# Kernel tuning notes

Hardware: AMD Instinct MI355X
Metric: run time of the kernel (lower is better)

## Reference

```python
import jax, jax.numpy as jnp
import numpy as np
import math

CHUNK = 128  # hardcoded chunk_size in the original module


def setup_inputs() -> dict:
    key = jax.random.key(0)
    ks = jax.random.split(key, 6)
    B, C, T, H, W = 8, 256, 16, 8, 8
    KC, VC = 8192, 512  # key_channels, value_channels (dk = KC/heads = T*H*W = 1024)
    return {
        "x": jax.random.normal(ks[0], (B, C, T, H, W), dtype=jnp.float32),
        "Wk": jax.random.normal(ks[1], (KC, C), dtype=jnp.float32) * 0.02,
        "Wq": jax.random.normal(ks[2], (KC, C), dtype=jnp.float32) * 0.02,
        "Wv": jax.random.normal(ks[3], (VC, C), dtype=jnp.float32) * 0.02,
        "Wr": jax.random.normal(ks[4], (C, VC), dtype=jnp.float32) * 0.02,
        "br": jnp.zeros((C,), dtype=jnp.float32),
        "num_heads": 8,
    }


def reference(x, Wk, Wq, Wv, Wr, br, num_heads):
    B, C, T, H, W = x.shape
    N = T * H * W
    # 1x1x1 Conv3d == per-position linear projection
    k = jnp.einsum('oc,bcthw->bothw', Wk, x).reshape(B, num_heads, -1, N)
    q = jnp.einsum('oc,bcthw->bothw', Wq, x).reshape(B, num_heads, -1, N)
    v = jnp.einsum('oc,bcthw->bothw', Wv, x).reshape(B, num_heads, -1, N)
    dk = k.shape[2]  # == N by structural constraint of the original matmul
    # matmul(keys, q_chunk) over all chunks at once (matmul is linear in q):
    # contracts keys' position axis with queries' channel axis, as in torch.
    scores = jnp.matmul(k, q) / math.sqrt(dk)  # [B, h, dk, N]
    # softmax applied per query-chunk of size CHUNK along the last axis
    nchunks = N // CHUNK
    attn = jax.nn.softmax(
        scores.reshape(B, num_heads, dk, nchunks, CHUNK), axis=-1
    ).reshape(B, num_heads, dk, N)
    out = jnp.matmul(v, attn)  # [B, h, dv, N] (dk == N)
    out = out.reshape(B, -1, T, H, W)
    out = jnp.einsum('oc,bcthw->bothw', Wr, out) + br[None, :, None, None, None]
    return out
```

## Files before the change

### kernel.cpp

```cpp
#include <hip/hip_runtime.h>
#include <hip/hip_bf16.h>


using bf16x8 = __attribute__((ext_vector_type(8))) __bf16;
using f32x4  = __attribute__((ext_vector_type(4))) float;
using s16x4  = __attribute__((ext_vector_type(4))) short;

static __device__ __forceinline__ short f2b(float f) {
  union { float f; unsigned u; } v; v.f = f;
  unsigned r = v.u + 0x7fffu + ((v.u >> 16) & 1u);
  return (short)(r >> 16);
}

static __device__ __forceinline__ void gll16(const void* g, void* l) {
  __builtin_amdgcn_global_load_lds(
      (const __attribute__((address_space(1))) void*)g,
      (__attribute__((address_space(3))) void*)l, 16, 0, 0);
}

#define MFMA16(a, b, c) __builtin_amdgcn_mfma_f32_16x16x32_bf16((a), (b), (c), 0, 0, 0)

__global__ __launch_bounds__(256) void cvt_bf16(const float* __restrict__ in,
                                                short* __restrict__ out, int n) {
  int i = (blockIdx.x * 256 + threadIdx.x) * 4;
  if (i >= n) return;
  float4 v = *(const float4*)(in + i);
  s16x4 s = { f2b(v.x), f2b(v.y), f2b(v.z), f2b(v.w) };
  *(s16x4*)(out + i) = s;
}

__global__ __launch_bounds__(256) void tcvt(const float* __restrict__ in,
    short* __restrict__ outP, short* __restrict__ outT,
    int R, int C, long inB, long pB, long tB)
{
  __shared__ short tile[64][68];
  long bz = blockIdx.z;
  const float* src = in + bz * inB;
  int r0 = blockIdx.y * 64, c0 = blockIdx.x * 64;
  int t = threadIdx.x;
  int r = t >> 2, cq = (t & 3) * 16;
  #pragma unroll
  for (int e = 0; e < 16; e += 4) {
    float4 v = *(const float4*)(&src[(long)(r0 + r) * C + (c0 + cq + e)]);
    s16x4 s = { f2b(v.x), f2b(v.y), f2b(v.z), f2b(v.w) };
    *(s16x4*)(&tile[r][cq + e]) = s;
    if (outP) *(s16x4*)(&outP[bz * pB + (long)(r0 + r) * C + (c0 + cq + e)]) = s;
  }
  __syncthreads();
  int tr = t >> 2, re = (t & 3) * 16;
  short tmp[16];
  #pragma unroll
  for (int e = 0; e < 16; ++e) tmp[e] = tile[re + e][tr];
  short* dst = &outT[bz * tB + (long)(c0 + tr) * R + (r0 + re)];
  #pragma unroll
  for (int e = 0; e < 16; e += 4) *(s16x4*)(&dst[e]) = *(const s16x4*)(&tmp[e]);
}

template<bool F32OUT>
__global__ __launch_bounds__(256) void gemm_nt(
    const short* __restrict__ A, const short* __restrict__ B,
    void* __restrict__ C, const float* __restrict__ bias,
    int M, int N, int K, int lda, int ldb, int ldc,
    long aSB, long aSH, long bSB, long bSH, long cSB, long cSH, int nh)
{
  int batch = blockIdx.z;
  int hb = batch % nh, bb = batch / nh;
  const short* Ab = A + bb * aSB + hb * aSH;
  const short* Bb = B + bb * bSB + hb * bSH;
  long cOff = bb * cSB + hb * cSH;
  int m0 = blockIdx.y * 128, n0 = blockIdx.x * 128;
  __shared__ short As[128 * 64];
  __shared__ short Bs[128 * 64];
  int t = threadIdx.x;
  int lane = t & 63, wid = t >> 6;
  int wm = (wid >> 1) * 64, wn = (wid & 1) * 64;
  int rl = lane & 15, q = lane >> 4;
  f32x4 acc[4][4] = {};
  for (int k0 = 0; k0 < K; k0 += 64) {
    __syncthreads();
    #pragma unroll
    for (int j = 0; j < 4; ++j) {
      int g = j * 256 + t;
      int r = g >> 3, cc = g & 7;
      int cs = cc ^ (r & 7);
      gll16(&Ab[(long)(m0 + r) * lda + k0 + cs * 8], (char*)As + (j * 256 + wid * 64) * 16);
      gll16(&Bb[(long)(n0 + r) * ldb + k0 + cs * 8], (char*)Bs + (j * 256 + wid * 64) * 16);
    }
    __syncthreads();
    #pragma unroll
    for (int kt = 0; kt < 2; ++kt) {
      int cq = kt * 4 + q;
      bf16x8 af[4], bfv[4];
      #pragma unroll
      for (int mi = 0; mi < 4; ++mi) {
        int R = wm + 16 * mi + rl;
        af[mi] = *(const bf16x8*)((const char*)As + (R * 8 + (cq ^ (R & 7))) * 16);
      }
      #pragma unroll
      for (int ni = 0; ni < 4; ++ni) {
        int RN = wn + 16 * ni + rl;
        bfv[ni] = *(const bf16x8*)((const char*)Bs + (RN * 8 + (cq ^ (RN & 7))) * 16);
      }
      #pragma unroll
      for (int mi = 0; mi < 4; ++mi)
        #pragma unroll
        for (int ni = 0; ni < 4; ++ni)
          acc[mi][ni] = MFMA16(af[mi], bfv[ni], acc[mi][ni]);
    }
  }
  #pragma unroll
  for (int mi = 0; mi < 4; ++mi)
    #pragma unroll
    for (int ni = 0; ni < 4; ++ni)
      #pragma unroll
      for (int r = 0; r < 4; ++r) {
        int row = m0 + wm + 16 * mi + 4 * q + r;
        int col = n0 + wn + 16 * ni + rl;
        float val = acc[mi][ni][r];
        if (F32OUT) {
          ((float*)C)[cOff + (long)row * ldc + col] = val + (bias ? bias[row] : 0.f);
        } else {
          ((short*)C)[cOff + (long)row * ldc + col] = f2b(val);
        }
      }
}

__global__ __launch_bounds__(256, 1) void attn_fused(
    const short* __restrict__ Wk, const short* __restrict__ GT,
    const short* __restrict__ V, short* __restrict__ OT)
{
  __shared__ short smem[65536];
  short* Bs  = smem;
  short* Ab0 = smem + 32768;
  short* Ab1 = smem + 40960;
  short* aT  = smem + 49152;
  int blk = blockIdx.x;
  int c = blk & 7, h = (blk >> 3) & 7, b = blk >> 6;
  int t = threadIdx.x, lane = t & 63, w = t >> 6;
  int rl = lane & 15, q = lane >> 4;
  const short* Wkh = Wk + (long)(h * 1024) * 256;
  const short* GTc = GT + ((long)(b * 8 + h) * 1024 + c * 128) * 256;
  const short* Vb  = V + (long)(b * 512 + h * 64) * 1024;
  f32x4 ot[2][4] = {};
  const float SC = 1.4426950408889634f / 32.0f;

  #pragma unroll
  for (int j = 0; j < 16; ++j) {
    int g = j * 256 + t;
    int r = g >> 5, cc = g & 31;
    int cs = cc ^ (r & 7);
    gll16(&GTc[(long)r * 256 + cs * 8], (char*)Bs + (j * 256 + w * 64) * 16);
  }
  {
    #pragma unroll
    for (int j = 0; j < 4; ++j) {
      int g = j * 256 + t;
      int r = g >> 2, cc = g & 3;
      int cs = cc ^ ((r >> 1) & 3);
      gll16(&Wkh[(long)r * 256 + cs * 8], (char*)Ab0 + (j * 256 + w * 64) * 16);
    }
  }
  __syncthreads();

  short* Acur = Ab0;
  short* Anxt = Ab1;
  for (int o = 0; o < 4; ++o) {
    f32x4 s[4][8] = {};
    for (int k0i = 0; k0i < 8; ++k0i) {
      int k0 = k0i * 32;
      int nRow = -1, nK = 0;
      if (k0i < 7)      { nRow = o * 256;      nK = k0 + 32; }
      else if (o < 3)   { nRow = (o + 1) * 256; nK = 0; }
      if (nRow >= 0) {
        #pragma unroll
        for (int j = 0; j < 4; ++j) {
          int g = j * 256 + t;
          int r = g >> 2, cc = g & 3;
          int cs = cc ^ ((r >> 1) & 3);
          gll16(&Wkh[(long)(nRow + r) * 256 + nK + cs * 8],
                (char*)Anxt + (j * 256 + w * 64) * 16);
        }
      }
      bf16x8 af[4], bv[8];
      #pragma unroll
      for (int mi = 0; mi < 4; ++mi) {
        int R = w * 64 + 16 * mi + rl;
        af[mi] = *(const bf16x8*)((const char*)Acur + (R * 4 + (q ^ ((R >> 1) & 3))) * 16);
      }
      #pragma unroll
      for (int ni = 0; ni < 8; ++ni) {
        int Rj = 16 * ni + rl;
        int cb = (k0 >> 3) + q;
        bv[ni] = *(const bf16x8*)((const char*)Bs + (Rj * 32 + (cb ^ (Rj & 7))) * 16);
      }
      #pragma unroll
      for (int mi = 0; mi < 4; ++mi)
        #pragma unroll
        for (int ni = 0; ni < 8; ++ni)
          s[mi][ni] = MFMA16(af[mi], bv[ni], s[mi][ni]);
      __syncthreads();
      short* tmp = Acur; Acur = Anxt; Anxt = tmp;
    }
    float mx[4][4], sm[4][4], rc[4][4];
    #pragma unroll
    for (int mi = 0; mi < 4; ++mi)
      #pragma unroll
      for (int r = 0; r < 4; ++r) {
        float m = s[mi][0][r];
        #pragma unroll
        for (int ni = 1; ni < 8; ++ni) m = fmaxf(m, s[mi][ni][r]);
        mx[mi][r] = m;
      }
    #pragma unroll
    for (int msk = 1; msk < 16; msk <<= 1)
      #pragma unroll
      for (int mi = 0; mi < 4; ++mi)
        #pragma unroll
        for (int r = 0; r < 4; ++r)
          mx[mi][r] = fmaxf(mx[mi][r], __shfl_xor(mx[mi][r], msk, 64));
    #pragma unroll
    for (int mi = 0; mi < 4; ++mi)
      #pragma unroll
      for (int r = 0; r < 4; ++r) sm[mi][r] = 0.f;
    #pragma unroll
    for (int mi = 0; mi < 4; ++mi)
      #pragma unroll
      for (int ni = 0; ni < 8; ++ni)
        #pragma unroll
        for (int r = 0; r < 4; ++r) {
          float p = exp2f((s[mi][ni][r] - mx[mi][r]) * SC);
          s[mi][ni][r] = p;
          sm[mi][r] += p;
        }
    #pragma unroll
    for (int msk = 1; msk < 16; msk <<= 1)
      #pragma unroll
      for (int mi = 0; mi < 4; ++mi)
        #pragma unroll
        for (int r = 0; r < 4; ++r)
          sm[mi][r] += __shfl_xor(sm[mi][r], msk, 64);
    #pragma unroll
    for (int mi = 0; mi < 4; ++mi)
      #pragma unroll
      for (int r = 0; r < 4; ++r) rc[mi][r] = __builtin_amdgcn_rcpf(sm[mi][r]);

    #pragma unroll
    for (int hf = 0; hf < 2; ++hf) {
      if ((w >> 1) == hf) {
        #pragma unroll
        for (int mi = 0; mi < 4; ++mi)
          #pragma unroll
          for (int ni = 0; ni < 8; ++ni) {
            s16x4 pk = { f2b(s[mi][ni][0] * rc[mi][0]), f2b(s[mi][ni][1] * rc[mi][1]),
                         f2b(s[mi][ni][2] * rc[mi][2]), f2b(s[mi][ni][3] * rc[mi][3]) };
            int j  = 16 * ni + rl;
            int ci = (w & 1) * 8 + 2 * mi + (q >> 1);
            *(s16x4*)((char*)aT + j * 256 + (ci ^ (j & 7)) * 16 + (q & 1) * 8) = pk;
          }
      }
      __syncthreads();
      #pragma unroll
      for (int kt = 0; kt < 4; ++kt) {
        bf16x8 pa[2], vv[4];
        #pragma unroll
        for (int mi = 0; mi < 2; ++mi) {
          int Rj = 32 * w + 16 * mi + rl;
          int ci = kt * 4 + q;
          pa[mi] = *(const bf16x8*)((const char*)aT + Rj * 256 + (ci ^ (Rj & 7)) * 16);
        }
        int ig = o * 256 + hf * 128 + kt * 32 + q * 8;
        #pragma unroll
        for (int nd = 0; nd < 4; ++nd)
          vv[nd] = *(const bf16x8*)(&Vb[(long)(16 * nd + rl) * 1024 + ig]);
        #pragma unroll
        for (int mi = 0; mi < 2; ++mi)
          #pragma unroll
          for (int nd = 0; nd < 4; ++nd)
            ot[mi][nd] = MFMA16(pa[mi], vv[nd], ot[mi][nd]);
      }
      __syncthreads();
    }
  }
  short* OTb = OT + (long)(b * 1024 + c * 128) * 512 + h * 64;
  #pragma unroll
  for (int mi = 0; mi < 2; ++mi)
    #pragma unroll
    for (int nd = 0; nd < 4; ++nd)
      #pragma unroll
      for (int r = 0; r < 4; ++r) {
        int j = 32 * w + 16 * mi + 4 * q + r;
        int d = 16 * nd + rl;
        OTb[(long)j * 512 + d] = f2b(ot[mi][nd][r]);
      }
}

extern "C" void kernel_launch(void* const* d_in, const int* in_sizes, int n_in,
                              void* d_out, int out_size, void* d_ws, size_t ws_size,
                              hipStream_t stream)
{
  const float* x  = (const float*)d_in[0];
  const float* Wk = (const float*)d_in[1];
  const float* Wq = (const float*)d_in[2];
  const float* Wv = (const float*)d_in[3];
  const float* Wr = (const float*)d_in[4];
  const float* br = (const float*)d_in[5];
  float* out = (float*)d_out;

  char* ws = (char*)d_ws;
  short* Xbf = (short*)(ws + 0);
  short* XT  = (short*)(ws + 4194304);
  short* WqT = (short*)(ws + 8388608);
  short* Wkb = (short*)(ws + 12582912);
  short* Wvb = (short*)(ws + 16777216);
  short* Wrb = (short*)(ws + 17039360);
  short* Mb  = (short*)(ws + 17301504);
  short* GTb = (short*)(ws + 25690112);
  short* Vbf = (short*)(ws + 59244544);
  short* OTb = (short*)(ws + 67633152);

  tcvt<<<dim3(16, 4, 8), 256, 0, stream>>>(x, Xbf, XT, 256, 1024, 262144L, 262144L, 262144L);
  tcvt<<<dim3(4, 128, 1), 256, 0, stream>>>(Wq, nullptr, WqT, 8192, 256, 0L, 0L, 0L);
  cvt_bf16<<<2048, 256, 0, stream>>>(Wk, Wkb, 2097152);
  cvt_bf16<<<128, 256, 0, stream>>>(Wv, Wvb, 131072);
  cvt_bf16<<<128, 256, 0, stream>>>(Wr, Wrb, 131072);

  gemm_nt<false><<<dim3(2, 2, 64), 256, 0, stream>>>(Xbf, WqT, Mb, nullptr,
      256, 256, 1024, 1024, 8192, 256,
      262144L, 0L, 0L, 1024L, 524288L, 65536L, 8);
  gemm_nt<false><<<dim3(2, 8, 64), 256, 0, stream>>>(XT, Mb, GTb, nullptr,
      1024, 256, 256, 256, 256, 256,
      262144L, 0L, 524288L, 65536L, 2097152L, 262144L, 8);
  gemm_nt<false><<<dim3(8, 4, 8), 256, 0, stream>>>(Wvb, XT, Vbf, nullptr,
      512, 1024, 256, 256, 256, 1024,
      0L, 0L, 262144L, 0L, 524288L, 0L, 1);
  attn_fused<<<512, 256, 0, stream>>>(Wkb, GTb, Vbf, OTb);
  gemm_nt<true><<<dim3(8, 2, 8), 256, 0, stream>>>(Wrb, OTb, out, br,
      256, 1024, 512, 512, 512, 1024,
      0L, 0L, 524288L, 0L, 262144L, 0L, 1);
}
```

Baseline: 291.4 us.

## Stream GT tiles in double-buffered K slices to cut LDS and allow two blocks per CU

Measured after the change: 295.8 us. About the same (+1.5%).

```diff
diff --git a/kernel.cpp b/kernel.cpp
--- a/kernel.cpp
+++ b/kernel.cpp
@@ -125,15 +125,16 @@
       }
 }
 
-__global__ __launch_bounds__(256, 1) void attn_fused(
+__global__ __launch_bounds__(256, 2) void attn_fused(
     const short* __restrict__ Wk, const short* __restrict__ GT,
     const short* __restrict__ V, short* __restrict__ OT)
 {
-  __shared__ short smem[65536];
-  short* Bs  = smem;
-  short* Ab0 = smem + 32768;
-  short* Ab1 = smem + 40960;
-  short* aT  = smem + 49152;
+  __shared__ short smem[40960];
+  short* As0 = smem;
+  short* As1 = smem + 8192;
+  short* Bs0 = smem + 16384;
+  short* Bs1 = smem + 20480;
+  short* aT  = smem + 24576;
   int blk = blockIdx.x;
   int c = blk & 7, h = (blk >> 3) & 7, b = blk >> 6;
   int t = threadIdx.x, lane = t & 63, w = t >> 6;
@@ -144,62 +145,56 @@
   f32x4 ot[2][4] = {};
   const float SC = 1.4426950408889634f / 32.0f;
 
-  #pragma unroll
-  for (int j = 0; j < 16; ++j) {
-    int g = j * 256 + t;
-    int r = g >> 5, cc = g & 31;
-    int cs = cc ^ (r & 7);
-    gll16(&GTc[(long)r * 256 + cs * 8], (char*)Bs + (j * 256 + w * 64) * 16);
-  }
-  {
+  auto stageA = [&](short* dst, int oRow, int k0) {
     #pragma unroll
     for (int j = 0; j < 4; ++j) {
       int g = j * 256 + t;
       int r = g >> 2, cc = g & 3;
       int cs = cc ^ ((r >> 1) & 3);
-      gll16(&Wkh[(long)r * 256 + cs * 8], (char*)Ab0 + (j * 256 + w * 64) * 16);
-    }
-  }
+      gll16(&Wkh[(long)(oRow + r) * 256 + k0 + cs * 8],
+            (char*)dst + (j * 256 + w * 64) * 16);
+    }
+  };
+  auto stageB = [&](short* dst, int k0) {
+    #pragma unroll
+    for (int j = 0; j < 2; ++j) {
+      int g = j * 256 + t;
+      int r = g >> 2, cc = g & 3;
+      int cs = cc ^ ((r >> 1) & 3);
+      gll16(&GTc[(long)r * 256 + k0 + cs * 8],
+            (char*)dst + (j * 256 + w * 64) * 16);
+    }
+  };
+
+  short *Ac = As0, *An = As1, *Bc = Bs0, *Bn = Bs1;
+  stageA(Ac, 0, 0);
+  stageB(Bc, 0);
   __syncthreads();
 
-  short* Acur = Ab0;
-  short* Anxt = Ab1;
   for (int o = 0; o < 4; ++o) {
     f32x4 s[4][8] = {};
-    for (int k0i = 0; k0i < 8; ++k0i) {
-      int k0 = k0i * 32;
-      int nRow = -1, nK = 0;
-      if (k0i < 7)      { nRow = o * 256;      nK = k0 + 32; }
-      else if (o < 3)   { nRow = (o + 1) * 256; nK = 0; }
-      if (nRow >= 0) {
-        #pragma unroll
-        for (int j = 0; j < 4; ++j) {
-          int g = j * 256 + t;
-          int r = g >> 2, cc = g & 3;
-          int cs = cc ^ ((r >> 1) & 3);
-          gll16(&Wkh[(long)(nRow + r) * 256 + nK + cs * 8],
-                (char*)Anxt + (j * 256 + w * 64) * 16);
-        }
-      }
-      bf16x8 af[4], bv[8];
+    for (int sl = 0; sl < 8; ++sl) {
+      int ns = sl + 1, no = o;
+      if (ns == 8) { ns = 0; no = o + 1; }
+      if (no < 4) { stageA(An, no * 256, ns * 32); stageB(Bn, ns * 32); }
+      bf16x8 af[4];
       #pragma unroll
       for (int mi = 0; mi < 4; ++mi) {
         int R = w * 64 + 16 * mi + rl;
-        af[mi] = *(const bf16x8*)((const char*)Acur + (R * 4 + (q ^ ((R >> 1) & 3))) * 16);
+        af[mi] = *(const bf16x8*)((const char*)Ac + (R * 4 + (q ^ ((R >> 1) & 3))) * 16);
       }
       #pragma unroll
       for (int ni = 0; ni < 8; ++ni) {
         int Rj = 16 * ni + rl;
-        int cb = (k0 >> 3) + q;
-        bv[ni] = *(const bf16x8*)((const char*)Bs + (Rj * 32 + (cb ^ (Rj & 7))) * 16);
-      }
-      #pragma unroll
-      for (int mi = 0; mi < 4; ++mi)
-        #pragma unroll
-        for (int ni = 0; ni < 8; ++ni)
-          s[mi][ni] = MFMA16(af[mi], bv[ni], s[mi][ni]);
+        bf16x8 bv = *(const bf16x8*)((const char*)Bc + (Rj * 4 + (q ^ ((Rj >> 1) & 3))) * 16);
+        #pragma unroll
+        for (int mi = 0; mi < 4; ++mi)
+          s[mi][ni] = MFMA16(af[mi], bv, s[mi][ni]);
+      }
       __syncthreads();
-      short* tmp = Acur; Acur = Anxt; Anxt = tmp;
+      short* tp;
+      tp = Ac; Ac = An; An = tp;
+      tp = Bc; Bc = Bn; Bn = tp;
     }
     float mx[4][4], sm[4][4], rc[4][4];
     #pragma unroll
```

## Split attention over key-row quarters with fp32 atomic accumulation and smaller GEMM tiles

Applied to the files above, without the earlier changes.

Measured after the change: 314.1 us. +7.8%, slower.

```diff
diff --git a/kernel.cpp b/kernel.cpp
--- a/kernel.cpp
+++ b/kernel.cpp
@@ -20,10 +20,16 @@
 
 #define MFMA16(a, b, c) __builtin_amdgcn_mfma_f32_16x16x32_bf16((a), (b), (c), 0, 0, 0)
 
-__global__ __launch_bounds__(256) void cvt_bf16(const float* __restrict__ in,
-                                                short* __restrict__ out, int n) {
-  int i = (blockIdx.x * 256 + threadIdx.x) * 4;
-  if (i >= n) return;
+__global__ __launch_bounds__(256) void cvt3(
+    const float* __restrict__ wk, short* __restrict__ wko,
+    const float* __restrict__ wv, short* __restrict__ wvo,
+    const float* __restrict__ wr, short* __restrict__ wro) {
+  int bx = blockIdx.x;
+  const float* in; short* out; int base;
+  if (bx < 2048)      { in = wk; out = wko; base = bx; }
+  else if (bx < 2176) { in = wv; out = wvo; base = bx - 2048; }
+  else                { in = wr; out = wro; base = bx - 2176; }
+  int i = base * 1024 + threadIdx.x * 4;
   float4 v = *(const float4*)(in + i);
   s16x4 s = { f2b(v.x), f2b(v.y), f2b(v.z), f2b(v.w) };
   *(s16x4*)(out + i) = s;
@@ -56,43 +62,50 @@
   for (int e = 0; e < 16; e += 4) *(s16x4*)(&dst[e]) = *(const s16x4*)(&tmp[e]);
 }
 
-template<bool F32OUT>
+template<int BM, bool F32OUT>
 __global__ __launch_bounds__(256) void gemm_nt(
     const short* __restrict__ A, const short* __restrict__ B,
     void* __restrict__ C, const float* __restrict__ bias,
     int M, int N, int K, int lda, int ldb, int ldc,
     long aSB, long aSH, long bSB, long bSH, long cSB, long cSH, int nh)
 {
+  constexpr int MI = BM / 32;
   int batch = blockIdx.z;
   int hb = batch % nh, bb = batch / nh;
   const short* Ab = A + bb * aSB + hb * aSH;
   const short* Bb = B + bb * bSB + hb * bSH;
   long cOff = bb * cSB + hb * cSH;
-  int m0 = blockIdx.y * 128, n0 = blockIdx.x * 128;
-  __shared__ short As[128 * 64];
+  int m0 = blockIdx.y * BM, n0 = blockIdx.x * 128;
+  __shared__ short As[BM * 64];
   __shared__ short Bs[128 * 64];
   int t = threadIdx.x;
   int lane = t & 63, wid = t >> 6;
-  int wm = (wid >> 1) * 64, wn = (wid & 1) * 64;
+  int wm = (wid >> 1) * (BM / 2), wn = (wid & 1) * 64;
   int rl = lane & 15, q = lane >> 4;
-  f32x4 acc[4][4] = {};
+  f32x4 acc[MI][4] = {};
   for (int k0 = 0; k0 < K; k0 += 64) {
     __syncthreads();
+    #pragma unroll
+    for (int j = 0; j < BM / 32; ++j) {
+      int g = j * 256 + t;
+      int r = g >> 3, cc = g & 7;
+      int cs = cc ^ (r & 7);
+      gll16(&Ab[(long)(m0 + r) * lda + k0 + cs * 8], (char*)As + (j * 256 + wid * 64) * 16);
+    }
     #pragma unroll
     for (int j = 0; j < 4; ++j) {
       int g = j * 256 + t;
       int r = g >> 3, cc = g & 7;
       int cs = cc ^ (r & 7);
-      gll16(&Ab[(long)(m0 + r) * lda + k0 + cs * 8], (char*)As + (j * 256 + wid * 64) * 16);
       gll16(&Bb[(long)(n0 + r) * ldb + k0 + cs * 8], (char*)Bs + (j * 256 + wid * 64) * 16);
     }
     __syncthreads();
     #pragma unroll
     for (int kt = 0; kt < 2; ++kt) {
       int cq = kt * 4 + q;
-      bf16x8 af[4], bfv[4];
-      #pragma unroll
-      for (int mi = 0; mi < 4; ++mi) {
+      bf16x8 af[MI], bfv[4];
+      #pragma unroll
+      for (int mi = 0; mi < MI; ++mi) {
         int R = wm + 16 * mi + rl;
         af[mi] = *(const bf16x8*)((const char*)As + (R * 8 + (cq ^ (R & 7))) * 16);
       }
@@ -102,14 +115,14 @@
         bfv[ni] = *(const bf16x8*)((const char*)Bs + (RN * 8 + (cq ^ (RN & 7))) * 16);
       }
       #pragma unroll
-      for (int mi = 0; mi < 4; ++mi)
+      for (int mi = 0; mi < MI; ++mi)
         #pragma unroll
         for (int ni = 0; ni < 4; ++ni)
           acc[mi][ni] = MFMA16(af[mi], bfv[ni], acc[mi][ni]);
     }
   }
   #pragma unroll
-  for (int mi = 0; mi < 4; ++mi)
+  for (int mi = 0; mi < MI; ++mi)
     #pragma unroll
     for (int ni = 0; ni < 4; ++ni)
       #pragma unroll
@@ -125,173 +138,175 @@
       }
 }
 
-__global__ __launch_bounds__(256, 1) void attn_fused(
+__global__ __launch_bounds__(256) void zero_o(float* __restrict__ lo,
+                                              float* __restrict__ hi) {
+  int z = blockIdx.y;
+  float* oz = (z < 48) ? lo + (long)z * 65536 : hi + (long)(z - 48) * 65536;
+  int idx = (blockIdx.x * 256 + threadIdx.x) * 4;
+  float4 zz = {0.f, 0.f, 0.f, 0.f};
+  *(float4*)(oz + idx) = zz;
+}
+
+__global__ __launch_bounds__(256) void qk_pv(
     const short* __restrict__ Wk, const short* __restrict__ GT,
-    const short* __restrict__ V, short* __restrict__ OT)
-{
-  __shared__ short smem[65536];
-  short* Bs  = smem;
-  short* Ab0 = smem + 32768;
-  short* Ab1 = smem + 40960;
-  short* aT  = smem + 49152;
-  int blk = blockIdx.x;
-  int c = blk & 7, h = (blk >> 3) & 7, b = blk >> 6;
+    const short* __restrict__ V, float* __restrict__ o32lo,
+    float* __restrict__ o32hi)
+{
+  __shared__ short smem[24576];
+  short* As = smem;
+  short* Bs = smem + 16384;
+  short* aT = smem;
+  int wg = blockIdx.x;
+  int c = wg & 7, b = (wg >> 3) & 7, ih = (wg >> 6) & 3, h = wg >> 8;
+  int z = b * 8 + h;
   int t = threadIdx.x, lane = t & 63, w = t >> 6;
   int rl = lane & 15, q = lane >> 4;
-  const short* Wkh = Wk + (long)(h * 1024) * 256;
-  const short* GTc = GT + ((long)(b * 8 + h) * 1024 + c * 128) * 256;
-  const short* Vb  = V + (long)(b * 512 + h * 64) * 1024;
-  f32x4 ot[2][4] = {};
+  const short* Ab = Wk + (long)(h * 1024 + ih * 256) * 256;
+  const short* Bb = GT + ((long)z * 1024 + c * 128) * 256;
+  const short* Vb = V + (long)(b * 512 + h * 64) * 1024;
+  float* Oz = (z < 48) ? o32lo + (long)z * 65536 : o32hi + (long)(z - 48) * 65536;
   const float SC = 1.4426950408889634f / 32.0f;
 
-  #pragma unroll
-  for (int j = 0; j < 16; ++j) {
-    int g = j * 256 + t;
-    int r = g >> 5, cc = g & 31;
-    int cs = cc ^ (r & 7);
-    gll16(&GTc[(long)r * 256 + cs * 8], (char*)Bs + (j * 256 + w * 64) * 16);
-  }
-  {
+  f32x4 s[4][8] = {};
+  for (int k0 = 0; k0 < 256; k0 += 64) {
+    __syncthreads();
+    #pragma unroll
+    for (int j = 0; j < 8; ++j) {
+      int g = j * 256 + t;
+      int r = g >> 3, cc = g & 7, cs = cc ^ (r & 7);
+      gll16(&Ab[(long)r * 256 + k0 + cs * 8], (char*)As + (j * 256 + w * 64) * 16);
+    }
     #pragma unroll
     for (int j = 0; j < 4; ++j) {
       int g = j * 256 + t;
-      int r = g >> 2, cc = g & 3;
-      int cs = cc ^ ((r >> 1) & 3);
-      gll16(&Wkh[(long)r * 256 + cs * 8], (char*)Ab0 + (j * 256 + w * 64) * 16);
+      int r = g >> 3, cc = g & 7, cs = cc ^ (r & 7);
+      gll16(&Bb[(long)r * 256 + k0 + cs * 8], (char*)Bs + (j * 256 + w * 64) * 16);
+    }
+    __syncthreads();
+    #pragma unroll
+    for (int kt = 0; kt < 2; ++kt) {
+      int cq = kt * 4 + q;
+      bf16x8 af[4];
+      #pragma unroll
+      for (int mi = 0; mi < 4; ++mi) {
+        int R = w * 64 + 16 * mi + rl;
+        af[mi] = *(const bf16x8*)((const char*)As + (R * 8 + (cq ^ (R & 7))) * 16);
+      }
+      #pragma unroll
+      for (int ni = 0; ni < 8; ++ni) {
+        int RN = 16 * ni + rl;
+        bf16x8 bv = *(const bf16x8*)((const char*)Bs + (RN * 8 + (cq ^ (RN & 7))) * 16);
+        #pragma unroll
+        for (int mi = 0; mi < 4; ++mi)
+          s[mi][ni] = MFMA16(af[mi], bv, s[mi][ni]);
+      }
     }
   }
   __syncthreads();
 
-  short* Acur = Ab0;
-  short* Anxt = Ab1;
-  for (int o = 0; o < 4; ++o) {
-    f32x4 s[4][8] = {};
-    for (int k0i = 0; k0i < 8; ++k0i) {
-      int k0 = k0i * 32;
-      int nRow = -1, nK = 0;
-      if (k0i < 7)      { nRow = o * 256;      nK = k0 + 32; }
-      else if (o < 3)   { nRow = (o + 1) * 256; nK = 0; }
-      if (nRow >= 0) {
-        #pragma unroll
-        for (int j = 0; j < 4; ++j) {
-          int g = j * 256 + t;
-          int r = g >> 2, cc = g & 3;
-          int cs = cc ^ ((r >> 1) & 3);
-          gll16(&Wkh[(long)(nRow + r) * 256 + nK + cs * 8],
-                (char*)Anxt + (j * 256 + w * 64) * 16);
-        }
-      }
-      bf16x8 af[4], bv[8];
-      #pragma unroll
-      for (int mi = 0; mi < 4; ++mi) {
-        int R = w * 64 + 16 * mi + rl;
-        af[mi] = *(const bf16x8*)((const char*)Acur + (R * 4 + (q ^ ((R >> 1) & 3))) * 16);
-      }
-      #pragma unroll
-      for (int ni = 0; ni < 8; ++ni) {
-        int Rj = 16 * ni + rl;
-        int cb = (k0 >> 3) + q;
-        bv[ni] = *(const bf16x8*)((const char*)Bs + (Rj * 32 + (cb ^ (Rj & 7))) * 16);
-      }
+  float mx[4][4], sm[4][4], rc[4][4];
+  #pragma unroll
+  for (int mi = 0; mi < 4; ++mi)
+    #pragma unroll
+    for (int r = 0; r < 4; ++r) {
+      float m = s[mi][0][r];
+      #pragma unroll
+      for (int ni = 1; ni < 8; ++ni) m = fmaxf(m, s[mi][ni][r]);
+      mx[mi][r] = m;
+    }
+  #pragma unroll
+  for (int msk = 1; msk < 16; msk <<= 1)
+    #pragma unroll
+    for (int mi = 0; mi < 4; ++mi)
+      #pragma unroll
+      for (int r = 0; r < 4; ++r)
+        mx[mi][r] = fmaxf(mx[mi][r], __shfl_xor(mx[mi][r], msk, 64));
+  #pragma unroll
+  for (int mi = 0; mi < 4; ++mi)
+    #pragma unroll
+    for (int r = 0; r < 4; ++r) sm[mi][r] = 0.f;
+  #pragma unroll
+  for (int mi = 0; mi < 4; ++mi)
+    #pragma unroll
+    for (int ni = 0; ni < 8; ++ni)
+      #pragma unroll
+      for (int r = 0; r < 4; ++r) {
+        float p = exp2f((s[mi][ni][r] - mx[mi][r]) * SC);
+        s[mi][ni][r] = p;
+        sm[mi][r] += p;
+      }
+  #pragma unroll
+  for (int msk = 1; msk < 16; msk <<= 1)
+    #pragma unroll
+    for (int mi = 0; mi < 4; ++mi)
+      #pragma unroll
+      for (int r = 0; r < 4; ++r)
+        sm[mi][r] += __shfl_xor(sm[mi][r], msk, 64);
+  #pragma unroll
+  for (int mi = 0; mi < 4; ++mi)
+    #pragma unroll
+    for (int r = 0; r < 4; ++r) rc[mi][r] = __builtin_amdgcn_rcpf(sm[mi][r]);
+
+  f32x4 ot[2][4] = {};
+  #pragma unroll
+  for (int hf = 0; hf < 2; ++hf) {
+    if ((w >> 1) == hf) {
       #pragma unroll
       for (int mi = 0; mi < 4; ++mi)
         #pragma unroll
-        for (int ni = 0; ni < 8; ++ni)
-          s[mi][ni] = MFMA16(af[mi], bv[ni], s[mi][ni]);
-      __syncthreads();
-      short* tmp = Acur; Acur = Anxt; Anxt = tmp;
-    }
-    float mx[4][4], sm[4][4], rc[4][4];
-    #pragma unroll
-    for (int mi = 0; mi < 4; ++mi)
-      #pragma unroll
-      for (int r = 0; r < 4; ++r) {
-        float m = s[mi][0][r];
-        #pragma unroll
-        for (int ni = 1; ni < 8; ++ni) m = fmaxf(m, s[mi][ni][r]);
-        mx[mi][r] = m;
-      }
-    #pragma unroll
-    for (int msk = 1; msk < 16; msk <<= 1)
-      #pragma unroll
-      for (int mi = 0; mi < 4; ++mi)
-        #pragma unroll
-        for (int r = 0; r < 4; ++r)
-          mx[mi][r] = fmaxf(mx[mi][r], __shfl_xor(mx[mi][r], msk, 64));
-    #pragma unroll
-    for (int mi = 0; mi < 4; ++mi)
-      #pragma unroll
-      for (int r = 0; r < 4; ++r) sm[mi][r] = 0.f;
-    #pragma unroll
-    for (int mi = 0; mi < 4; ++mi)
-      #pragma unroll
-      for (int ni = 0; ni < 8; ++ni)
-        #pragma unroll
-        for (int r = 0; r < 4; ++r) {
-          float p = exp2f((s[mi][ni][r] - mx[mi][r]) * SC);
-          s[mi][ni][r] = p;
-          sm[mi][r] += p;
+        for (int ni = 0; ni < 8; ++ni) {
+          s16x4 pk = { f2b(s[mi][ni][0] * rc[mi][0]), f2b(s[mi][ni][1] * rc[mi][1]),
+                       f2b(s[mi][ni][2] * rc[mi][2]), f2b(s[mi][ni][3] * rc[mi][3]) };
+          int j  = 16 * ni + rl;
+          int ci = (w & 1) * 8 + 2 * mi + (q >> 1);
+          *(s16x4*)((char*)aT + j * 256 + (ci ^ (j & 7)) * 16 + (q & 1) * 8) = pk;
         }
-    #pragma unroll
-    for (int msk = 1; msk < 16; msk <<= 1)
-      #pragma unroll
-      for (int mi = 0; mi < 4; ++mi)
-        #pragma unroll
-        for (int r = 0; r < 4; ++r)
-          sm[mi][r] += __shfl_xor(sm[mi][r], msk, 64);
-    #pragma unroll
-    for (int mi = 0; mi < 4; ++mi)
-      #pragma unroll
-      for (int r = 0; r < 4; ++r) rc[mi][r] = __builtin_amdgcn_rcpf(sm[mi][r]);
-
-    #pragma unroll
-    for (int hf = 0; hf < 2; ++hf) {
-      if ((w >> 1) == hf) {
-        #pragma unroll
-        for (int mi = 0; mi < 4; ++mi)
-          #pragma unroll
-          for (int ni = 0; ni < 8; ++ni) {
-            s16x4 pk = { f2b(s[mi][ni][0] * rc[mi][0]), f2b(s[mi][ni][1] * rc[mi][1]),
-                         f2b(s[mi][ni][2] * rc[mi][2]), f2b(s[mi][ni][3] * rc[mi][3]) };
-            int j  = 16 * ni + rl;
-            int ci = (w & 1) * 8 + 2 * mi + (q >> 1);
-            *(s16x4*)((char*)aT + j * 256 + (ci ^ (j & 7)) * 16 + (q & 1) * 8) = pk;
-          }
-      }
-      __syncthreads();
-      #pragma unroll
-      for (int kt = 0; kt < 4; ++kt) {
-        bf16x8 pa[2], vv[4];
-        #pragma unroll
-        for (int mi = 0; mi < 2; ++mi) {
-          int Rj = 32 * w + 16 * mi + rl;
-          int ci = kt * 4 + q;
-          pa[mi] = *(const bf16x8*)((const char*)aT + Rj * 256 + (ci ^ (Rj & 7)) * 16);
-        }
-        int ig = o * 256 + hf * 128 + kt * 32 + q * 8;
+    }
+    __syncthreads();
+    #pragma unroll
+    for (int kt = 0; kt < 4; ++kt) {
+      bf16x8 pa[2], vv[4];
+      #pragma unroll
+      for (int mi = 0; mi < 2; ++mi) {
+        int Rj = 32 * w + 16 * mi + rl;
+        int ci = kt * 4 + q;
+        pa[mi] = *(const bf16x8*)((const char*)aT + Rj * 256 + (ci ^ (Rj & 7)) * 16);
+      }
+      int ig = ih * 256 + hf * 128 + kt * 32 + q * 8;
+      #pragma unroll
+      for (int nd = 0; nd < 4; ++nd)
+        vv[nd] = *(const bf16x8*)(&Vb[(long)(16 * nd + rl) * 1024 + ig]);
+      #pragma unroll
+      for (int mi = 0; mi < 2; ++mi)
         #pragma unroll
         for (int nd = 0; nd < 4; ++nd)
-          vv[nd] = *(const bf16x8*)(&Vb[(long)(16 * nd + rl) * 1024 + ig]);
-        #pragma unroll
-        for (int mi = 0; mi < 2; ++mi)
-          #pragma unroll
-          for (int nd = 0; nd < 4; ++nd)
-            ot[mi][nd] = MFMA16(pa[mi], vv[nd], ot[mi][nd]);
-      }
-      __syncthreads();
-    }
+          ot[mi][nd] = MFMA16(pa[mi], vv[nd], ot[mi][nd]);
+    }
+    __syncthreads();
   }
-  short* OTb = OT + (long)(b * 1024 + c * 128) * 512 + h * 64;
   #pragma unroll
   for (int mi = 0; mi < 2; ++mi)
     #pragma unroll
     for (int nd = 0; nd < 4; ++nd)
       #pragma unroll
       for (int r = 0; r < 4; ++r) {
-        int j = 32 * w + 16 * mi + 4 * q + r;
+        int j = c * 128 + 32 * w + 16 * mi + 4 * q + r;
         int d = 16 * nd + rl;
-        OTb[(long)j * 512 + d] = f2b(ot[mi][nd][r]);
-      }
+        atomicAdd(&Oz[(long)j * 64 + d], ot[mi][nd][r]);
+      }
+}
+
+__global__ __launch_bounds__(256) void cvt_o(const float* __restrict__ lo,
+    const float* __restrict__ hi, short* __restrict__ OT)
+{
+  int z = blockIdx.y;
+  const float* oz = (z < 48) ? lo + (long)z * 65536 : hi + (long)(z - 48) * 65536;
+  int b = z >> 3, h = z & 7;
+  int off = (blockIdx.x * 256 + threadIdx.x) * 4;
+  int j = off >> 6, d = off & 63;
+  float4 v = *(const float4*)(oz + off);
+  s16x4 s = { f2b(v.x), f2b(v.y), f2b(v.z), f2b(v.w) };
+  *(s16x4*)(&OT[((long)b * 1024 + j) * 512 + h * 64 + d]) = s;
 }
 
 extern "C" void kernel_launch(void* const* d_in, const int* in_sizes, int n_in,
@@ -318,23 +333,28 @@
   short* Vbf = (short*)(ws + 59244544);
   short* OTb = (short*)(ws + 67633152);
 
+  float* o32lo = (float*)(ws + 0);
+  float* o32hi = (float*)(ws + 17301504);
+
   tcvt<<<dim3(16, 4, 8), 256, 0, stream>>>(x, Xbf, XT, 256, 1024, 262144L, 262144L, 262144L);
   tcvt<<<dim3(4, 128, 1), 256, 0, stream>>>(Wq, nullptr, WqT, 8192, 256, 0L, 0L, 0L);
-  cvt_bf16<<<2048, 256, 0, stream>>>(Wk, Wkb, 2097152);
-  cvt_bf16<<<128, 256, 0, stream>>>(Wv, Wvb, 131072);
-  cvt_bf16<<<128, 256, 0, stream>>>(Wr, Wrb, 131072);
-
-  gemm_nt<false><<<dim3(2, 2, 64), 256, 0, stream>>>(Xbf, WqT, Mb, nullptr,
+  cvt3<<<2304, 256, 0, stream>>>(Wk, Wkb, Wv, Wvb, Wr, Wrb);
+
+  gemm_nt<64, false><<<dim3(2, 4, 64), 256, 0, stream>>>(Xbf, WqT, Mb, nullptr,
       256, 256, 1024, 1024, 8192, 256,
       262144L, 0L, 0L, 1024L, 524288L, 65536L, 8);
-  gemm_nt<false><<<dim3(2, 8, 64), 256, 0, stream>>>(XT, Mb, GTb, nullptr,
+  gemm_nt<128, false><<<dim3(2, 8, 64), 256, 0, stream>>>(XT, Mb, GTb, nullptr,
       1024, 256, 256, 256, 256, 256,
       262144L, 0L, 524288L, 65536L, 2097152L, 262144L, 8);
-  gemm_nt<false><<<dim3(8, 4, 8), 256, 0, stream>>>(Wvb, XT, Vbf, nullptr,
+  gemm_nt<64, false><<<dim3(8, 8, 8), 256, 0, stream>>>(Wvb, XT, Vbf, nullptr,
       512, 1024, 256, 256, 256, 1024,
       0L, 0L, 262144L, 0L, 524288L, 0L, 1);
-  attn_fused<<<512, 256, 0, stream>>>(Wkb, GTb, Vbf, OTb);
-  gemm_nt<true><<<dim3(8, 2, 8), 256, 0, stream>>>(Wrb, OTb, out, br,
+
+  zero_o<<<dim3(64, 64), 256, 0, stream>>>(o32lo, o32hi);
+  qk_pv<<<2048, 256, 0, stream>>>(Wkb, GTb, Vbf, o32lo, o32hi);
+  cvt_o<<<dim3(64, 64), 256, 0, stream>>>(o32lo, o32hi, OTb);
+
+  gemm_nt<64, true><<<dim3(8, 4, 8), 256, 0, stream>>>(Wrb, OTb, out, br,
       256, 1024, 512, 512, 512, 1024,
       0L, 0L, 524288L, 0L, 262144L, 0L, 1);
 }
```
